# Kernel optimization log

Hardware: AMD Instinct MI355X
Metric: run time of the kernel (lower is better)

Reference implementation:

```python
import math
import jax, jax.numpy as jnp
import numpy as np

B = 16; ENC_S = 64; ENC_T = 96
SCALE = 64; POOL = 16; DM = 256; NH = 16
E_LAYERS = 3; D_LAYERS = 2; DFF = 1024
OUT_S = 64; OUT_T = 32
LN_EPS = 1e-5


def _pe(d_model, length):
    pos = np.arange(length, dtype=np.float32)[:, None]
    div = np.exp(np.arange(0, d_model, 2, dtype=np.float32) * (-math.log(10000.0) / d_model))
    pe = np.zeros((length, d_model), np.float32)
    pe[:, 0::2] = np.sin(pos * div)
    pe[:, 1::2] = np.cos(pos * div)
    return jnp.asarray(pe)


def _conv1d_circ(x, w, b):
    # x: (N, C, L), w: (O, C, 3); torch Conv1d(padding=1, padding_mode='circular')
    xp = jnp.pad(x, ((0, 0), (0, 0), (1, 1)), mode='wrap')
    y = jax.lax.conv_general_dilated(xp, w, (1,), 'VALID',
                                     dimension_numbers=('NCH', 'OIH', 'NCH'))
    return y + b[None, :, None]


def _layernorm(x, w, b):
    mu = jnp.mean(x, -1, keepdims=True)
    var = jnp.var(x, -1, keepdims=True)
    return (x - mu) * jax.lax.rsqrt(var + LN_EPS) * w + b


def _data_embedding(x, sproj_w, sproj_b, scproj_w, scproj_b, tok_w, tok_b):
    Bb = x.shape[0]
    h = _conv1d_circ(jnp.swapaxes(x, 1, 2), sproj_w, sproj_b)       # (B, enc_t, enc_t)
    h = _conv1d_circ(h, scproj_w, scproj_b)                          # (B, scale, enc_t)
    h = _conv1d_circ(jnp.swapaxes(h, 1, 2), scproj_w, scproj_b)     # (B, scale, scale)
    h = h.reshape(Bb * SCALE, 1, SCALE)
    tok = jnp.swapaxes(_conv1d_circ(h, tok_w, tok_b), 1, 2)          # (B*scale, scale, dm)
    emb = tok + _pe(DM, SCALE)[None]
    return emb.reshape(Bb, SCALE, SCALE, DM)


def _lin_attn(q, k, v, causal):
    # q,k,v: (Bp, L, H, E); k/v adaptively avg-pooled over L to POOL (L % POOL == 0)
    Bp, L, H, E = q.shape
    win = L // POOL
    kp = k.reshape(Bp, POOL, win, H, E).mean(axis=2)
    vp = v.reshape(Bp, POOL, win, H, E).mean(axis=2)
    scores = jnp.einsum('blhe,bshe->bhls', q, kp)      # (Bp, H, L, POOL)
    if causal:
        m = jnp.arange(POOL)[None, :] > jnp.arange(L)[:, None]
        scores = jnp.where(m[None, None], -jnp.inf, scores)
    A = jax.nn.softmax(scores / math.sqrt(E), axis=-1)
    return jnp.einsum('bhls,bshd->blhd', A, vp)


def _st_attn(x, kv, Wq, bq, Wo, bo, causal):
    Bb, T, S, dm = x.shape
    H = NH // 2
    proj = lambda z: z @ Wq.T + bq
    # faithful to source: query_projection used for q, k AND v; views are flat reshapes
    qt = proj(x.reshape(Bb * S, T, dm)).reshape(Bb * S, T, H, -1)
    qs = proj(x.reshape(Bb * T, S, dm)).reshape(Bb * T, S, H, -1)
    kt = proj(kv.reshape(Bb * S, T, dm)).reshape(Bb * S, T, H, -1)
    ks = proj(kv.reshape(Bb * T, S, dm)).reshape(Bb * T, S, H, -1)
    out_t = _lin_attn(qt, kt, kt, causal).reshape(Bb, S, T, -1)
    out_s = _lin_attn(qs, ks, ks, causal).reshape(Bb, S, T, -1)
    out = jnp.concatenate([out_t, out_s], axis=-1).reshape(Bb, S * T, 2 * dm)
    out = out @ Wo.T + bo
    return out.reshape(Bb, T, S, dm)


def _ffn(x, c1w, c1b, c2w, c2b):
    # conv1d kernel_size=1 over the T axis of (B*S, T, dm) == pointwise GEMM
    Bb, T, S, dm = x.shape
    y = x.reshape(Bb * S, T, dm)
    y = jax.nn.gelu(jnp.einsum('ntd,fd->ntf', y, c1w) + c1b, approximate=False)
    y = jnp.einsum('ntf,df->ntd', y, c2w) + c2b
    return y.reshape(Bb, T, S, dm)


def _forward(x_enc, x_dec,
             enc_sproj_w, enc_sproj_b, enc_scproj_w, enc_scproj_b, enc_tok_w, enc_tok_b,
             dec_sproj_w, dec_sproj_b, dec_scproj_w, dec_scproj_b, dec_tok_w, dec_tok_b,
             e_Wq, e_bq, e_Wo, e_bo, e_c1w, e_c1b, e_c2w, e_c2b,
             e_ln1w, e_ln1b, e_ln2w, e_ln2b, enc_norm_w, enc_norm_b,
             d_sWq, d_sbq, d_sWo, d_sbo, d_cWq, d_cbq, d_cWo, d_cbo,
             d_c1w, d_c1b, d_c2w, d_c2b,
             d_ln1w, d_ln1b, d_ln2w, d_ln2b, d_ln3w, d_ln3b,
             dec_norm_w, dec_norm_b, proj_w, proj_b):
    enc = _data_embedding(x_enc, enc_sproj_w, enc_sproj_b, enc_scproj_w, enc_scproj_b, enc_tok_w, enc_tok_b)
    for i in range(E_LAYERS):
        h = enc + _st_attn(enc, enc, e_Wq[i], e_bq[i], e_Wo[i], e_bo[i], False)
        h = _layernorm(h, e_ln1w[i], e_ln1b[i])
        enc = _layernorm(h + _ffn(h, e_c1w[i], e_c1b[i], e_c2w[i], e_c2b[i]), e_ln2w[i], e_ln2b[i])
    enc = _layernorm(enc, enc_norm_w, enc_norm_b)
    dec = _data_embedding(x_dec, dec_sproj_w, dec_sproj_b, dec_scproj_w, dec_scproj_b, dec_tok_w, dec_tok_b)
    for i in range(D_LAYERS):
        h = dec + _st_attn(dec, dec, d_sWq[i], d_sbq[i], d_sWo[i], d_sbo[i], True)
        h = _layernorm(h, d_ln1w[i], d_ln1b[i])
        h = h + _st_attn(h, enc, d_cWq[i], d_cbq[i], d_cWo[i], d_cbo[i], False)
        h = _layernorm(h, d_ln2w[i], d_ln2b[i])
        dec = _layernorm(h + _ffn(h, d_c1w[i], d_c1b[i], d_c2w[i], d_c2b[i]), d_ln3w[i], d_ln3b[i])
    dec = _layernorm(dec, dec_norm_w, dec_norm_b)
    dec = dec.mean(axis=2)                 # (B, scale, dm)
    out = dec @ proj_w.T + proj_b          # (B, scale, out_s)
    return out[:, -OUT_T:, :]


def setup_inputs() -> dict:
    keys = iter(jax.random.split(jax.random.key(0), 80))
    def nrm(shape, s=0.02):
        return jax.random.normal(next(keys), shape, jnp.float32) * s
    E, D = E_LAYERS, D_LAYERS
    inp = {
        'x_enc': nrm((B, ENC_T, ENC_S), 1.0),
        'x_dec': nrm((B, ENC_T, ENC_S), 1.0),
    }
    for p in ('enc', 'dec'):
        inp[p + '_sproj_w'] = nrm((ENC_T, ENC_S, 3)); inp[p + '_sproj_b'] = nrm((ENC_T,))
        inp[p + '_scproj_w'] = nrm((SCALE, ENC_T, 3)); inp[p + '_scproj_b'] = nrm((SCALE,))
        inp[p + '_tok_w'] = nrm((DM, 1, 3), 0.1); inp[p + '_tok_b'] = nrm((DM,))
    inp.update(
        e_Wq=nrm((E, DM, DM)), e_bq=nrm((E, DM)),
        e_Wo=nrm((E, DM, 2 * DM)), e_bo=nrm((E, DM)),
        e_c1w=nrm((E, DFF, DM)), e_c1b=nrm((E, DFF)),
        e_c2w=nrm((E, DM, DFF)), e_c2b=nrm((E, DM)),
        e_ln1w=jnp.ones((E, DM)), e_ln1b=jnp.zeros((E, DM)),
        e_ln2w=jnp.ones((E, DM)), e_ln2b=jnp.zeros((E, DM)),
        enc_norm_w=jnp.ones((DM,)), enc_norm_b=jnp.zeros((DM,)),
        d_sWq=nrm((D, DM, DM)), d_sbq=nrm((D, DM)),
        d_sWo=nrm((D, DM, 2 * DM)), d_sbo=nrm((D, DM)),
        d_cWq=nrm((D, DM, DM)), d_cbq=nrm((D, DM)),
        d_cWo=nrm((D, DM, 2 * DM)), d_cbo=nrm((D, DM)),
        d_c1w=nrm((D, DFF, DM)), d_c1b=nrm((D, DFF)),
        d_c2w=nrm((D, DM, DFF)), d_c2b=nrm((D, DM)),
        d_ln1w=jnp.ones((D, DM)), d_ln1b=jnp.zeros((D, DM)),
        d_ln2w=jnp.ones((D, DM)), d_ln2b=jnp.zeros((D, DM)),
        d_ln3w=jnp.ones((D, DM)), d_ln3b=jnp.zeros((D, DM)),
        dec_norm_w=jnp.ones((DM,)), dec_norm_b=jnp.zeros((DM,)),
        proj_w=nrm((OUT_S, DM)), proj_b=nrm((OUT_S,)),
    )
    return inp


def reference(x_enc, x_dec,
              enc_sproj_w, enc_sproj_b, enc_scproj_w, enc_scproj_b, enc_tok_w, enc_tok_b,
              dec_sproj_w, dec_sproj_b, dec_scproj_w, dec_scproj_b, dec_tok_w, dec_tok_b,
              e_Wq, e_bq, e_Wo, e_bo, e_c1w, e_c1b, e_c2w, e_c2b,
              e_ln1w, e_ln1b, e_ln2w, e_ln2b, enc_norm_w, enc_norm_b,
              d_sWq, d_sbq, d_sWo, d_sbo, d_cWq, d_cbq, d_cWo, d_cbo,
              d_c1w, d_c1b, d_c2w, d_c2b,
              d_ln1w, d_ln1b, d_ln2w, d_ln2b, d_ln3w, d_ln3b,
              dec_norm_w, dec_norm_b, proj_w, proj_b):
    return _forward(x_enc, x_dec,
                    enc_sproj_w, enc_sproj_b, enc_scproj_w, enc_scproj_b, enc_tok_w, enc_tok_b,
                    dec_sproj_w, dec_sproj_b, dec_scproj_w, dec_scproj_b, dec_tok_w, dec_tok_b,
                    e_Wq, e_bq, e_Wo, e_bo, e_c1w, e_c1b, e_c2w, e_c2b,
                    e_ln1w, e_ln1b, e_ln2w, e_ln2b, enc_norm_w, enc_norm_b,
                    d_sWq, d_sbq, d_sWo, d_sbo, d_cWq, d_cbq, d_cWo, d_cbo,
                    d_c1w, d_c1b, d_c2w, d_c2b,
                    d_ln1w, d_ln1b, d_ln2w, d_ln2b, d_ln3w, d_ln3b,
                    dec_norm_w, dec_norm_b, proj_w, proj_b)
```

## Files before the change

kernel.cpp:

```cpp
#include <hip/hip_runtime.h>


typedef unsigned short u16;
typedef short s16;
typedef __attribute__((ext_vector_type(8))) s16 bfrag;
typedef __attribute__((ext_vector_type(4))) float f32x4;

__device__ __forceinline__ float b2f(u16 u) {
  union { float f; unsigned int i; } v; v.i = ((unsigned int)u) << 16; return v.f;
}
__device__ __forceinline__ u16 f2b(float f) {
  union { float f; unsigned int i; } v; v.f = f;
  unsigned int x = v.i;
  return (u16)((x + 0x7FFFu + ((x >> 16) & 1u)) >> 16);
}
__device__ __forceinline__ float gelu_f(float v) {
  float u = 0.7978845608f * v * (1.0f + 0.044715f * v * v);
  float e = __expf(2.0f * u);
  return v * (1.0f - 1.0f / (e + 1.0f));
}

__device__ __forceinline__ void gload16(const void* g, void* l) {
  __builtin_amdgcn_global_load_lds(
      (const __attribute__((address_space(1))) unsigned int*)g,
      (__attribute__((address_space(3))) unsigned int*)l, 16, 0, 0);
}

__global__ void ws_signal(float* out, float v) { out[0] = v; }

__global__ void cvt_bf(const float* __restrict__ src, u16* __restrict__ dst, int n) {
  int i = blockIdx.x * 256 + threadIdx.x;
  if (i < n) dst[i] = f2b(src[i]);
}
__global__ void weff_bf(const float* __restrict__ Wo, u16* __restrict__ W) {
  int n = blockIdx.x, k = threadIdx.x;
  W[n * 256 + k] = f2b(Wo[n * 512 + k] + Wo[n * 512 + 256 + k]);
}

__global__ void pe_kernel(float* __restrict__ pe) {
  int l = blockIdx.x, d = threadIdx.x;
  int i = d >> 1;
  float div = expf((float)(2 * i) * (-9.210340371976184f / 256.0f));
  float ang = (float)l * div;
  pe[l * 256 + d] = (d & 1) ? cosf(ang) : sinf(ang);
}

__global__ void conv_sproj(const float* __restrict__ x, const float* __restrict__ w,
                           const float* __restrict__ bias, float* __restrict__ h1) {
  int o = blockIdx.x, b = blockIdx.y, l = threadIdx.x;
  const float* wo = w + o * 192;
  const float* xb = x + (size_t)b * 96 * 64;
  float acc = bias[o];
#pragma unroll
  for (int k = 0; k < 3; ++k) {
    int lp = l + k - 1; if (lp < 0) lp += 96; if (lp >= 96) lp -= 96;
    const float* xr = xb + lp * 64;
    for (int c = 0; c < 64; ++c) acc = fmaf(xr[c], wo[c * 3 + k], acc);
  }
  h1[((size_t)b * 96 + o) * 96 + l] = acc;
}

__global__ void conv_scproj_t(const float* __restrict__ h1, const float* __restrict__ w,
                              const float* __restrict__ bias, float* __restrict__ h2) {
  int o = blockIdx.x, b = blockIdx.y, l = threadIdx.x;
  const float* wo = w + o * 288;
  const float* hb = h1 + (size_t)b * 96 * 96;
  float acc = bias[o];
#pragma unroll
  for (int k = 0; k < 3; ++k) {
    int lp = l + k - 1; if (lp < 0) lp += 96; if (lp >= 96) lp -= 96;
    for (int c = 0; c < 96; ++c) acc = fmaf(hb[c * 96 + lp], wo[c * 3 + k], acc);
  }
  h2[((size_t)b * 64 + o) * 96 + l] = acc;
}

__global__ void conv_scproj_s(const float* __restrict__ h2, const float* __restrict__ w,
                              const float* __restrict__ bias, float* __restrict__ h3) {
  int o = blockIdx.x, b = blockIdx.y, l = threadIdx.x;
  const float* wo = w + o * 288;
  const float* hb = h2 + (size_t)b * 64 * 96;
  float acc = bias[o];
#pragma unroll
  for (int k = 0; k < 3; ++k) {
    int lp = l + k - 1; if (lp < 0) lp += 64; if (lp >= 64) lp -= 64;
    for (int c = 0; c < 96; ++c) acc = fmaf(hb[lp * 96 + c], wo[c * 3 + k], acc);
  }
  h3[((size_t)b * 64 + o) * 64 + l] = acc;
}

__global__ void tok_embed(const float* __restrict__ h3, const float* __restrict__ w,
                          const float* __restrict__ bias, const float* __restrict__ pe,
                          u16* __restrict__ E) {
  int g = blockIdx.x, d = threadIdx.x;
  __shared__ float row[64];
  if (d < 64) row[d] = h3[(size_t)g * 64 + d];
  __syncthreads();
  float w0 = w[d * 3], w1 = w[d * 3 + 1], w2 = w[d * 3 + 2], bd = bias[d];
  for (int j = 0; j < 64; ++j) {
    int jm = (j + 63) & 63, jp = (j + 1) & 63;
    float v = bd + row[jm] * w0 + row[j] * w1 + row[jp] * w2 + pe[j * 256 + d];
    E[((size_t)g * 64 + j) * 256 + d] = f2b(v);
  }
}

template <int ACT, int NBX>
__global__ __launch_bounds__(256) void mfma_gemm(const u16* __restrict__ A,
                                                 const u16* __restrict__ W,
                                                 const float* __restrict__ bias,
                                                 u16* __restrict__ C, int N, int K,
                                                 int nby) {
  __shared__ s16 smem[16384];
  s16* A0 = smem;        s16* A1 = smem + 4096;
  s16* B0 = smem + 8192; s16* B1 = smem + 12288;
  constexpr int LB = (NBX == 8) ? 3 : 1;
  int f = blockIdx.x;
  int q = (NBX * nby) >> 3;
  int w = (f & 7) * q + (f >> 3);
  int bx = w & (NBX - 1), by = w >> LB;
  int t = threadIdx.x;
  int wave = t >> 6, lane = t & 63;
  int wr = wave >> 1, wc = wave & 1;
  int row0 = by * 128, col0 = bx * 128;
  int kc = (lane >> 4) & 3, rr = lane & 15;
  const u16* Ap0 = A + (size_t)(row0 + wave * 16 + rr) * K + kc * 8;
  const u16* Ap1 = A + (size_t)(row0 + (wave + 4) * 16 + rr) * K + kc * 8;
  const u16* Bp0 = W + (size_t)(col0 + wave * 16 + rr) * K + kc * 8;
  const u16* Bp1 = W + (size_t)(col0 + (wave + 4) * 16 + rr) * K + kc * 8;
  f32x4 acc[4][4];
#pragma unroll
  for (int m = 0; m < 4; ++m)
#pragma unroll
    for (int n = 0; n < 4; ++n) acc[m][n] = (f32x4){0.f, 0.f, 0.f, 0.f};

  auto STAGE = [&](s16* a, s16* b, int kidx) {
    int k0 = kidx * 32;
    gload16(Ap0 + k0, a + wave * 512);
    gload16(Ap1 + k0, a + (wave + 4) * 512);
    gload16(Bp0 + k0, b + wave * 512);
    gload16(Bp1 + k0, b + (wave + 4) * 512);
  };
  int nk = K >> 5;
  auto STEP = [&](const s16* a, const s16* b, s16* sa, s16* sb, int ks) {
    if (ks + 1 < nk) asm volatile("s_waitcnt vmcnt(4)" ::: "memory");
    else             asm volatile("s_waitcnt vmcnt(0)" ::: "memory");
    __builtin_amdgcn_sched_barrier(0);
    __builtin_amdgcn_s_barrier();
    __builtin_amdgcn_sched_barrier(0);
    bfrag af[4], bf[4];
#pragma unroll
    for (int m = 0; m < 4; ++m) af[m] = *(const bfrag*)(a + ((wr * 4 + m) * 64 + lane) * 8);
#pragma unroll
    for (int n = 0; n < 4; ++n) bf[n] = *(const bfrag*)(b + ((wc * 4 + n) * 64 + lane) * 8);
    asm volatile("s_waitcnt lgkmcnt(0)" ::: "memory");
    __builtin_amdgcn_sched_barrier(0);
    __builtin_amdgcn_s_barrier();
    __builtin_amdgcn_sched_barrier(0);
    if (ks + 2 < nk) STAGE(sa, sb, ks + 2);
#pragma unroll
    for (int m = 0; m < 4; ++m)
#pragma unroll
      for (int n = 0; n < 4; ++n)
        acc[m][n] = __builtin_amdgcn_mfma_f32_16x16x32_bf16(af[m], bf[n], acc[m][n], 0, 0, 0);
  };

  STAGE(A0, B0, 0);
  STAGE(A1, B1, 1);
  for (int ks = 0; ks < nk; ks += 2) {
    STEP(A0, B0, A0, B0, ks);
    STEP(A1, B1, A1, B1, ks + 1);
  }
  s16* Cs = smem;
  int g4 = (lane >> 4) << 2;
  int cl = lane & 15;
  float bc[4];
#pragma unroll
  for (int n = 0; n < 4; ++n) bc[n] = bias[col0 + wc * 64 + n * 16 + cl];
#pragma unroll
  for (int P = 0; P < 4; ++P) {
    __syncthreads();
    if (wr == (P >> 1)) {
#pragma unroll
      for (int mm = 0; mm < 2; ++mm) {
        int m = (P & 1) * 2 + mm;
#pragma unroll
        for (int n = 0; n < 4; ++n) {
#pragma unroll
          for (int r = 0; r < 4; ++r) {
            float v = acc[m][n][r] + bc[n];
            if (ACT == 1) v = gelu_f(v);
            Cs[(mm * 16 + g4 + r) * 136 + wc * 64 + n * 16 + cl] = (s16)f2b(v);
          }
        }
      }
    }
    __syncthreads();
#pragma unroll
    for (int it = 0; it < 2; ++it) {
      int idx = it * 256 + t;
      int lr = idx >> 4, slot = idx & 15;
      *(uint4*)(C + (size_t)(row0 + P * 32 + lr) * N + col0 + slot * 8) =
          *(const uint4*)(Cs + lr * 136 + slot * 8);
    }
  }
}

__global__ __launch_bounds__(512) void mfma_gemm_resln(const u16* __restrict__ X,
                                                       const u16* __restrict__ W,
                                                       const float* __restrict__ bias,
                                                       u16* __restrict__ R,
                                                       const float* __restrict__ lnw,
                                                       const float* __restrict__ lnb,
                                                       int K) {
  __shared__ s16 smem[24576];
  __shared__ float pls[32][4][2];
  s16* A0 = smem;        s16* A1 = smem + 4096;
  s16* B0 = smem + 8192; s16* B1 = smem + 16384;
  int t = threadIdx.x;
  int wave = t >> 6, lane = t & 63;
  int wr = wave >> 2, wc = wave & 3;
  int row0 = blockIdx.x * 128;
  int kc = (lane >> 4) & 3, rr = lane & 15;
  const u16* Xp = X + (size_t)(row0 + wave * 16 + rr) * K + kc * 8;
  const u16* Wp0 = W + (size_t)(wave * 16 + rr) * K + kc * 8;
  const u16* Wp1 = W + (size_t)((wave + 8) * 16 + rr) * K + kc * 8;
  f32x4 acc[4][4];
#pragma unroll
  for (int m = 0; m < 4; ++m)
#pragma unroll
    for (int n = 0; n < 4; ++n) acc[m][n] = (f32x4){0.f, 0.f, 0.f, 0.f};

  auto STAGE = [&](s16* a, s16* b, int kidx) {
    int k0 = kidx * 32;
    gload16(Xp + k0, a + wave * 512);
    gload16(Wp0 + k0, b + wave * 512);
    gload16(Wp1 + k0, b + (wave + 8) * 512);
  };
  int nk = K >> 5;
  auto STEP = [&](const s16* a, const s16* b, s16* sa, s16* sb, int ks) {
    if (ks + 1 < nk) asm volatile("s_waitcnt vmcnt(3)" ::: "memory");
    else             asm volatile("s_waitcnt vmcnt(0)" ::: "memory");
    __builtin_amdgcn_sched_barrier(0);
    __builtin_amdgcn_s_barrier();
    __builtin_amdgcn_sched_barrier(0);
    bfrag af[4], bf[4];
#pragma unroll
    for (int m = 0; m < 4; ++m) af[m] = *(const bfrag*)(a + ((wr * 4 + m) * 64 + lane) * 8);
#pragma unroll
    for (int n = 0; n < 4; ++n) bf[n] = *(const bfrag*)(b + ((wc * 4 + n) * 64 + lane) * 8);
    asm volatile("s_waitcnt lgkmcnt(0)" ::: "memory");
    __builtin_amdgcn_sched_barrier(0);
    __builtin_amdgcn_s_barrier();
    __builtin_amdgcn_sched_barrier(0);
    if (ks + 2 < nk) STAGE(sa, sb, ks + 2);
#pragma unroll
    for (int m = 0; m < 4; ++m)
#pragma unroll
      for (int n = 0; n < 4; ++n)
        acc[m][n] = __builtin_amdgcn_mfma_f32_16x16x32_bf16(af[m], bf[n], acc[m][n], 0, 0, 0);
  };

  STAGE(A0, B0, 0);
  STAGE(A1, B1, 1);
  for (int ks = 0; ks < nk; ks += 2) {
    STEP(A0, B0, A0, B0, ks);
    STEP(A1, B1, A1, B1, ks + 1);
  }
  s16* Rs = smem;
  int g4 = (lane >> 4) << 2;
  int cl = lane & 15;
  float lw[4], lb[4], bc[4];
#pragma unroll
  for (int n = 0; n < 4; ++n) {
    int col = wc * 64 + n * 16 + cl;
    bc[n] = bias[col]; lw[n] = lnw[col]; lb[n] = lnb[col];
  }
#pragma unroll
  for (int P = 0; P < 4; ++P) {
    bool own = (wr == (P >> 1));
    __syncthreads();
#pragma unroll
    for (int it = 0; it < 2; ++it) {
      int idx = it * 512 + t;
      int lr = idx >> 5, slot = idx & 31;
      *(uint4*)(Rs + lr * 264 + slot * 8) =
          *(const uint4*)(R + (size_t)(row0 + P * 32 + lr) * 256 + slot * 8);
    }
    __syncthreads();
    if (own) {
#pragma unroll
      for (int mm = 0; mm < 2; ++mm) {
        int m = (P & 1) * 2 + mm;
#pragma unroll
        for (int r = 0; r < 4; ++r) {
          int lr = mm * 16 + g4 + r;
          float s = 0.f, s2 = 0.f;
#pragma unroll
          for (int n = 0; n < 4; ++n) {
            float v = acc[m][n][r] + bc[n] +
                      b2f((u16)Rs[lr * 264 + wc * 64 + n * 16 + cl]);
            acc[m][n][r] = v;
            s += v; s2 = fmaf(v, v, s2);
          }
#pragma unroll
          for (int o = 1; o < 16; o <<= 1) { s += __shfl_xor(s, o); s2 += __shfl_xor(s2, o); }
          if (cl == 0) { pls[lr][wc][0] = s; pls[lr][wc][1] = s2; }
        }
      }
    }
    __syncthreads();
    if (own) {
#pragma unroll
      for (int mm = 0; mm < 2; ++mm) {
        int m = (P & 1) * 2 + mm;
#pragma unroll
        for (int r = 0; r < 4; ++r) {
          int lr = mm * 16 + g4 + r;
          float s = pls[lr][0][0] + pls[lr][1][0] + pls[lr][2][0] + pls[lr][3][0];
          float s2 = pls[lr][0][1] + pls[lr][1][1] + pls[lr][2][1] + pls[lr][3][1];
          float mu = s * (1.0f / 256.0f);
          float var = fmaxf(s2 * (1.0f / 256.0f) - mu * mu, 0.0f);
          float rs = rsqrtf(var + 1e-5f);
#pragma unroll
          for (int n = 0; n < 4; ++n) {
            Rs[lr * 264 + wc * 64 + n * 16 + cl] =
                (s16)f2b((acc[m][n][r] - mu) * rs * lw[n] + lb[n]);
          }
        }
      }
    }
    __syncthreads();
#pragma unroll
    for (int it = 0; it < 2; ++it) {
      int idx = it * 512 + t;
      int lr = idx >> 5, slot = idx & 31;
      *(uint4*)(R + (size_t)(row0 + P * 32 + lr) * 256 + slot * 8) =
          *(const uint4*)(Rs + lr * 264 + slot * 8);
    }
  }
}

template <int CROSS, int CAUSAL>
__global__ __launch_bounds__(512) void lin_attn(u16* __restrict__ Q,
                                                const u16* __restrict__ KP) {
  __shared__ u16 qs[64 * 264];
  __shared__ float kpool[16][260];
  int p = blockIdx.x, t = threadIdx.x;
  u16* Qg = Q + (size_t)p * 16384;
#pragma unroll
  for (int i = 0; i < 4; ++i) {
    int idx = i * 512 + t;
    int row = idx >> 5, slot = idx & 31;
    *(uint4*)(qs + row * 264 + slot * 8) = *(const uint4*)(Qg + row * 256 + slot * 8);
  }
  __syncthreads();
  if (CROSS) {
    for (int idx = t; idx < 4096; idx += 512) {
      int s = idx >> 8, d = idx & 255;
      kpool[s][d] = b2f(KP[((size_t)p * 16 + s) * 256 + d]);
    }
  } else {
    for (int idx = t; idx < 4096; idx += 512) {
      int s = idx >> 8, d = idx & 255;
      const u16* b0 = qs + (4 * s) * 264 + d;
      kpool[s][d] = 0.25f * (b2f(b0[0]) + b2f(b0[264]) + b2f(b0[528]) + b2f(b0[792]));
    }
  }
  __syncthreads();
  int h = t >> 6, l = t & 63;
  u16* q = qs + l * 264 + h * 32;
  float qr[32];
#pragma unroll
  for (int e = 0; e < 32; e += 4) {
    ushort4 v = *(const ushort4*)&q[e];
    qr[e] = b2f(v.x); qr[e + 1] = b2f(v.y); qr[e + 2] = b2f(v.z); qr[e + 3] = b2f(v.w);
  }
  float sc[16], mx = -INFINITY;
#pragma unroll
  for (int s = 0; s < 16; ++s) {
    const float* kp = &kpool[s][h * 32];
    float d = 0.f;
#pragma unroll
    for (int e = 0; e < 32; ++e) d = fmaf(qr[e], kp[e], d);
    d *= 0.17677669529663687f;
    if (CAUSAL && s > l) d = -INFINITY;
    sc[s] = d; mx = fmaxf(mx, d);
  }
  float sum = 0.f;
#pragma unroll
  for (int s = 0; s < 16; ++s) { sc[s] = expf(sc[s] - mx); sum += sc[s]; }
  float inv = 1.0f / sum;
  float o[32] = {};
#pragma unroll
  for (int s = 0; s < 16; ++s) {
    float a = sc[s] * inv;
    const float* vp = &kpool[s][h * 32];
#pragma unroll
    for (int e = 0; e < 32; ++e) o[e] = fmaf(a, vp[e], o[e]);
  }
#pragma unroll
  for (int e = 0; e < 32; e += 4) {
    ushort4 v;
    v.x = f2b(o[e]); v.y = f2b(o[e + 1]); v.z = f2b(o[e + 2]); v.w = f2b(o[e + 3]);
    *(ushort4*)&q[e] = v;
  }
  __syncthreads();
#pragma unroll
  for (int i = 0; i < 4; ++i) {
    int idx = i * 512 + t;
    int row = idx >> 5, slot = idx & 31;
    *(uint4*)(Qg + row * 256 + slot * 8) = *(const uint4*)(qs + row * 264 + slot * 8);
  }
}

__global__ __launch_bounds__(256) void ln_bf(u16* __restrict__ X,
                                             const float* __restrict__ w,
                                             const float* __restrict__ b) {
  int lane = threadIdx.x & 63, wv = threadIdx.x >> 6;
  size_t row = (size_t)blockIdx.x * 4 + wv;
  size_t off = row * 256 + lane * 4;
  ushort4 xv = *(const ushort4*)(X + off);
  float v0 = b2f(xv.x), v1 = b2f(xv.y), v2 = b2f(xv.z), v3 = b2f(xv.w);
  float s = v0 + v1 + v2 + v3;
  float s2 = v0 * v0 + v1 * v1 + v2 * v2 + v3 * v3;
#pragma unroll
  for (int o = 32; o; o >>= 1) { s += __shfl_xor(s, o); s2 += __shfl_xor(s2, o); }
  float mu = s * (1.0f / 256.0f);
  float var = fmaxf(s2 * (1.0f / 256.0f) - mu * mu, 0.0f);
  float rs = rsqrtf(var + 1e-5f);
  float4 w4 = *(const float4*)(w + lane * 4);
  float4 b4 = *(const float4*)(b + lane * 4);
  ushort4 o4;
  o4.x = f2b((v0 - mu) * rs * w4.x + b4.x);
  o4.y = f2b((v1 - mu) * rs * w4.y + b4.y);
  o4.z = f2b((v2 - mu) * rs * w4.z + b4.z);
  o4.w = f2b((v3 - mu) * rs * w4.w + b4.w);
  *(ushort4*)(X + off) = o4;
}

__global__ void pool_bf(const u16* __restrict__ A, u16* __restrict__ P) {
  int r = blockIdx.x, d = threadIdx.x;
  int g = r >> 4, s = r & 15;
  const u16* src = A + ((size_t)g * 64 + 4 * (size_t)s) * 256 + d;
  float v = 0.25f * (b2f(src[0]) + b2f(src[256]) + b2f(src[512]) + b2f(src[768]));
  P[(size_t)r * 256 + d] = f2b(v);
}

__global__ __launch_bounds__(256) void mean_proj_bf(const u16* __restrict__ X,
                                                    const float* __restrict__ pw,
                                                    const float* __restrict__ pb,
                                                    float* __restrict__ out) {
  int bid = blockIdx.x;
  int b = bid >> 5, ii = bid & 31;
  int i = 32 + ii;
  __shared__ float md[256];
  int d = threadIdx.x;
  const u16* base = X + ((size_t)b * 64 + i) * 64 * 256 + d;
  float s = 0.f;
  for (int j = 0; j < 64; ++j) s += b2f(base[(size_t)j * 256]);
  md[d] = s * (1.0f / 64.0f);
  __syncthreads();
  if (d < 64) {
    float acc = pb[d];
    const float* wr = pw + d * 256;
    for (int k = 0; k < 256; ++k) acc = fmaf(md[k], wr[k], acc);
    out[((size_t)b * 32 + ii) * 64 + d] = acc;
  }
}

extern "C" void kernel_launch(void* const* d_in, const int* in_sizes, int n_in,
                              void* d_out, int out_size, void* d_ws, size_t ws_size,
                              hipStream_t stream) {
  (void)in_sizes; (void)out_size;
  if (n_in < 50) return;

  const float* x_enc = (const float*)d_in[0];
  const float* x_dec = (const float*)d_in[1];
  const float* enc_sproj_w = (const float*)d_in[2];
  const float* enc_sproj_b = (const float*)d_in[3];
  const float* enc_scproj_w = (const float*)d_in[4];
  const float* enc_scproj_b = (const float*)d_in[5];
  const float* enc_tok_w = (const float*)d_in[6];
  const float* enc_tok_b = (const float*)d_in[7];
  const float* dec_sproj_w = (const float*)d_in[8];
  const float* dec_sproj_b = (const float*)d_in[9];
  const float* dec_scproj_w = (const float*)d_in[10];
  const float* dec_scproj_b = (const float*)d_in[11];
  const float* dec_tok_w = (const float*)d_in[12];
  const float* dec_tok_b = (const float*)d_in[13];
  const float* e_Wq = (const float*)d_in[14];
  const float* e_bq = (const float*)d_in[15];
  const float* e_Wo = (const float*)d_in[16];
  const float* e_bo = (const float*)d_in[17];
  const float* e_c1w = (const float*)d_in[18];
  const float* e_c1b = (const float*)d_in[19];
  const float* e_c2w = (const float*)d_in[20];
  const float* e_c2b = (const float*)d_in[21];
  const float* e_ln1w = (const float*)d_in[22];
  const float* e_ln1b = (const float*)d_in[23];
  const float* e_ln2w = (const float*)d_in[24];
  const float* e_ln2b = (const float*)d_in[25];
  const float* enc_norm_w = (const float*)d_in[26];
  const float* enc_norm_b = (const float*)d_in[27];
  const float* d_sWq = (const float*)d_in[28];
  const float* d_sbq = (const float*)d_in[29];
  const float* d_sWo = (const float*)d_in[30];
  const float* d_sbo = (const float*)d_in[31];
  const float* d_cWq = (const float*)d_in[32];
  const float* d_cbq = (const float*)d_in[33];
  const float* d_cWo = (const float*)d_in[34];
  const float* d_cbo = (const float*)d_in[35];
  const float* d_c1w = (const float*)d_in[36];
  const float* d_c1b = (const float*)d_in[37];
  const float* d_c2w = (const float*)d_in[38];
  const float* d_c2b = (const float*)d_in[39];
  const float* d_ln1w = (const float*)d_in[40];
  const float* d_ln1b = (const float*)d_in[41];
  const float* d_ln2w = (const float*)d_in[42];
  const float* d_ln2b = (const float*)d_in[43];
  const float* d_ln3w = (const float*)d_in[44];
  const float* d_ln3b = (const float*)d_in[45];
  const float* dec_norm_w = (const float*)d_in[46];
  const float* dec_norm_b = (const float*)d_in[47];
  const float* proj_w = (const float*)d_in[48];
  const float* proj_b = (const float*)d_in[49];

  const size_t ACT = 16777216;
  const size_t POOLE = 4194304;
  const size_t WBN = 3538944;
  size_t base_need = (3 * ACT + 2 * POOLE + WBN) * 2 +
                     (size_t)(16384 + 147456 + 98304 + 65536) * 4;
  if (ws_size < base_need) {
    ws_signal<<<1, 1, 0, stream>>>((float*)d_out, (float)(ws_size >> 20));
    return;
  }
  char* wsb = (char*)d_ws;
  u16* A_enc = (u16*)wsb;  wsb += ACT * 2;
  u16* A_dec = (u16*)wsb;  wsb += ACT * 2;
  u16* T1 = (u16*)wsb;     wsb += ACT * 2;
  u16* PA = (u16*)wsb;     wsb += POOLE * 2;
  u16* PK = (u16*)wsb;     wsb += POOLE * 2;
  u16* WB = (u16*)wsb;     wsb += WBN * 2;
  float* PE = (float*)wsb;  wsb += 16384 * 4;
  float* EH1 = (float*)wsb; wsb += 147456 * 4;
  float* EH2 = (float*)wsb; wsb += 98304 * 4;
  float* EH3 = (float*)wsb; wsb += 65536 * 4;

  int hf_rows = 16384;
  u16* HF = T1;
  if (ws_size >= base_need + (size_t)65536 * 1024 * 2) {
    hf_rows = 65536; HF = (u16*)wsb;
  } else if (ws_size >= base_need + (size_t)32768 * 1024 * 2) {
    hf_rows = 32768; HF = (u16*)wsb;
  }

  u16* eWq = WB;
  u16* eWeff = WB + 196608;
  u16* eC1 = WB + 393216;
  u16* eC2 = WB + 1179648;
  u16* dB = WB + 1966080;
  u16* dsWq = dB;
  u16* dsWeff = dB + 131072;
  u16* dcWq = dB + 262144;
  u16* dcWeff = dB + 393216;
  u16* dC1 = dB + 524288;
  u16* dC2 = dB + 1048576;

  cvt_bf<<<768, 256, 0, stream>>>(e_Wq, eWq, 196608);
  cvt_bf<<<3072, 256, 0, stream>>>(e_c1w, eC1, 786432);
  cvt_bf<<<3072, 256, 0, stream>>>(e_c2w, eC2, 786432);
  cvt_bf<<<512, 256, 0, stream>>>(d_sWq, dsWq, 131072);
  cvt_bf<<<512, 256, 0, stream>>>(d_cWq, dcWq, 131072);
  cvt_bf<<<2048, 256, 0, stream>>>(d_c1w, dC1, 524288);
  cvt_bf<<<2048, 256, 0, stream>>>(d_c2w, dC2, 524288);
  for (int i = 0; i < 3; ++i)
    weff_bf<<<256, 256, 0, stream>>>(e_Wo + (size_t)i * 131072, eWeff + (size_t)i * 65536);
  for (int i = 0; i < 2; ++i) {
    weff_bf<<<256, 256, 0, stream>>>(d_sWo + (size_t)i * 131072, dsWeff + (size_t)i * 65536);
    weff_bf<<<256, 256, 0, stream>>>(d_cWo + (size_t)i * 131072, dcWeff + (size_t)i * 65536);
  }

  pe_kernel<<<64, 256, 0, stream>>>(PE);

  conv_sproj<<<dim3(96, 16), 96, 0, stream>>>(x_enc, enc_sproj_w, enc_sproj_b, EH1);
  conv_scproj_t<<<dim3(64, 16), 96, 0, stream>>>(EH1, enc_scproj_w, enc_scproj_b, EH2);
  conv_scproj_s<<<dim3(64, 16), 64, 0, stream>>>(EH2, enc_scproj_w, enc_scproj_b, EH3);
  tok_embed<<<1024, 256, 0, stream>>>(EH3, enc_tok_w, enc_tok_b, PE, A_enc);

  for (int i = 0; i < 3; ++i) {
    mfma_gemm<0, 2><<<1024, 256, 0, stream>>>(A_enc, eWq + (size_t)i * 65536,
                                              e_bq + i * 256, T1, 256, 256, 512);
    lin_attn<0, 0><<<1024, 512, 0, stream>>>(T1, nullptr);
    mfma_gemm_resln<<<512, 512, 0, stream>>>(T1, eWeff + (size_t)i * 65536, e_bo + i * 256,
                                             A_enc, e_ln1w + i * 256, e_ln1b + i * 256, 256);
    for (int m0 = 0; m0 < 65536; m0 += hf_rows) {
      u16* Xc = A_enc + (size_t)m0 * 256;
      int nby = hf_rows / 128;
      mfma_gemm<1, 8><<<8 * nby, 256, 0, stream>>>(
          Xc, eC1 + (size_t)i * 262144, e_c1b + i * 1024, HF, 1024, 256, nby);
      mfma_gemm_resln<<<nby, 512, 0, stream>>>(
          HF, eC2 + (size_t)i * 262144, e_c2b + i * 256, Xc,
          e_ln2w + i * 256, e_ln2b + i * 256, 1024);
    }
  }
  ln_bf<<<16384, 256, 0, stream>>>(A_enc, enc_norm_w, enc_norm_b);
  pool_bf<<<16384, 256, 0, stream>>>(A_enc, PA);

  conv_sproj<<<dim3(96, 16), 96, 0, stream>>>(x_dec, dec_sproj_w, dec_sproj_b, EH1);
  conv_scproj_t<<<dim3(64, 16), 96, 0, stream>>>(EH1, dec_scproj_w, dec_scproj_b, EH2);
  conv_scproj_s<<<dim3(64, 16), 64, 0, stream>>>(EH2, dec_scproj_w, dec_scproj_b, EH3);
  tok_embed<<<1024, 256, 0, stream>>>(EH3, dec_tok_w, dec_tok_b, PE, A_dec);

  for (int i = 0; i < 2; ++i) {
    mfma_gemm<0, 2><<<1024, 256, 0, stream>>>(A_dec, dsWq + (size_t)i * 65536,
                                              d_sbq + i * 256, T1, 256, 256, 512);
    lin_attn<0, 1><<<1024, 512, 0, stream>>>(T1, nullptr);
    mfma_gemm_resln<<<512, 512, 0, stream>>>(T1, dsWeff + (size_t)i * 65536, d_sbo + i * 256,
                                             A_dec, d_ln1w + i * 256, d_ln1b + i * 256, 256);
    mfma_gemm<0, 2><<<1024, 256, 0, stream>>>(A_dec, dcWq + (size_t)i * 65536,
                                              d_cbq + i * 256, T1, 256, 256, 512);
    mfma_gemm<0, 2><<<256, 256, 0, stream>>>(PA, dcWq + (size_t)i * 65536,
                                             d_cbq + i * 256, PK, 256, 256, 128);
    lin_attn<1, 0><<<1024, 512, 0, stream>>>(T1, PK);
    mfma_gemm_resln<<<512, 512, 0, stream>>>(T1, dcWeff + (size_t)i * 65536, d_cbo + i * 256,
                                             A_dec, d_ln2w + i * 256, d_ln2b + i * 256, 256);
    for (int m0 = 0; m0 < 65536; m0 += hf_rows) {
      u16* Xc = A_dec + (size_t)m0 * 256;
      int nby = hf_rows / 128;
      mfma_gemm<1, 8><<<8 * nby, 256, 0, stream>>>(
          Xc, dC1 + (size_t)i * 262144, d_c1b + i * 1024, HF, 1024, 256, nby);
      mfma_gemm_resln<<<nby, 512, 0, stream>>>(
          HF, dC2 + (size_t)i * 262144, d_c2b + i * 256, Xc,
          d_ln3w + i * 256, d_ln3b + i * 256, 1024);
    }
  }
  ln_bf<<<16384, 256, 0, stream>>>(A_dec, dec_norm_w, dec_norm_b);

  mean_proj_bf<<<512, 256, 0, stream>>>(A_dec, proj_w, proj_b, (float*)d_out);
}
```

Baseline: 1.792 ms.

## Restructure GEMM main loop to process K=64 per barrier step

```diff
diff --git a/kernel.cpp b/kernel.cpp
--- a/kernel.cpp
+++ b/kernel.cpp
@@ -109,9 +109,8 @@
                                                  const float* __restrict__ bias,
                                                  u16* __restrict__ C, int N, int K,
                                                  int nby) {
-  __shared__ s16 smem[16384];
-  s16* A0 = smem;        s16* A1 = smem + 4096;
-  s16* B0 = smem + 8192; s16* B1 = smem + 12288;
+  __shared__ s16 As[8192];
+  __shared__ s16 Bs[8192];
   constexpr int LB = (NBX == 8) ? 3 : 1;
   int f = blockIdx.x;
   int q = (NBX * nby) >> 3;
@@ -132,44 +131,53 @@
 #pragma unroll
     for (int n = 0; n < 4; ++n) acc[m][n] = (f32x4){0.f, 0.f, 0.f, 0.f};
 
-  auto STAGE = [&](s16* a, s16* b, int kidx) {
-    int k0 = kidx * 32;
+  auto STAGE32 = [&](s16* a, s16* b, int kidx32) {
+    int k0 = kidx32 * 32;
     gload16(Ap0 + k0, a + wave * 512);
     gload16(Ap1 + k0, a + (wave + 4) * 512);
     gload16(Bp0 + k0, b + wave * 512);
     gload16(Bp1 + k0, b + (wave + 4) * 512);
   };
-  int nk = K >> 5;
-  auto STEP = [&](const s16* a, const s16* b, s16* sa, s16* sb, int ks) {
-    if (ks + 1 < nk) asm volatile("s_waitcnt vmcnt(4)" ::: "memory");
-    else             asm volatile("s_waitcnt vmcnt(0)" ::: "memory");
+  auto STAGE64 = [&](int kidx64) {
+    STAGE32(As, Bs, kidx64 * 2);
+    STAGE32(As + 4096, Bs + 4096, kidx64 * 2 + 1);
+  };
+
+  int nk = K >> 6;
+  STAGE64(0);
+  for (int ks = 0; ks < nk; ++ks) {
+    asm volatile("s_waitcnt vmcnt(0)" ::: "memory");
     __builtin_amdgcn_sched_barrier(0);
     __builtin_amdgcn_s_barrier();
     __builtin_amdgcn_sched_barrier(0);
-    bfrag af[4], bf[4];
-#pragma unroll
-    for (int m = 0; m < 4; ++m) af[m] = *(const bfrag*)(a + ((wr * 4 + m) * 64 + lane) * 8);
-#pragma unroll
-    for (int n = 0; n < 4; ++n) bf[n] = *(const bfrag*)(b + ((wc * 4 + n) * 64 + lane) * 8);
+    bfrag al[4], bl[4], ah[4], bh[4];
+#pragma unroll
+    for (int m = 0; m < 4; ++m) {
+      al[m] = *(const bfrag*)(As + ((wr * 4 + m) * 64 + lane) * 8);
+      ah[m] = *(const bfrag*)(As + 4096 + ((wr * 4 + m) * 64 + lane) * 8);
+    }
+#pragma unroll
+    for (int n = 0; n < 4; ++n) {
+      bl[n] = *(const bfrag*)(Bs + ((wc * 4 + n) * 64 + lane) * 8);
+      bh[n] = *(const bfrag*)(Bs + 4096 + ((wc * 4 + n) * 64 + lane) * 8);
+    }
     asm volatile("s_waitcnt lgkmcnt(0)" ::: "memory");
     __builtin_amdgcn_sched_barrier(0);
     __builtin_amdgcn_s_barrier();
     __builtin_amdgcn_sched_barrier(0);
-    if (ks + 2 < nk) STAGE(sa, sb, ks + 2);
+    if (ks + 1 < nk) STAGE64(ks + 1);
 #pragma unroll
     for (int m = 0; m < 4; ++m)
 #pragma unroll
       for (int n = 0; n < 4; ++n)
-        acc[m][n] = __builtin_amdgcn_mfma_f32_16x16x32_bf16(af[m], bf[n], acc[m][n], 0, 0, 0);
-  };
-
-  STAGE(A0, B0, 0);
-  STAGE(A1, B1, 1);
-  for (int ks = 0; ks < nk; ks += 2) {
-    STEP(A0, B0, A0, B0, ks);
-    STEP(A1, B1, A1, B1, ks + 1);
-  }
-  s16* Cs = smem;
+        acc[m][n] = __builtin_amdgcn_mfma_f32_16x16x32_bf16(al[m], bl[n], acc[m][n], 0, 0, 0);
+#pragma unroll
+    for (int m = 0; m < 4; ++m)
+#pragma unroll
+      for (int n = 0; n < 4; ++n)
+        acc[m][n] = __builtin_amdgcn_mfma_f32_16x16x32_bf16(ah[m], bh[n], acc[m][n], 0, 0, 0);
+  }
+  s16* Cs = As;
   int g4 = (lane >> 4) << 2;
   int cl = lane & 15;
   float bc[4];
```

Result: slower. 1.840 ms (+2.7%).

## Fuse Q projection GEMM into linear attention and batch prologue kernels

Applied to the files above, without the earlier changes.

```diff
diff --git a/kernel.cpp b/kernel.cpp
--- a/kernel.cpp
+++ b/kernel.cpp
@@ -28,13 +28,30 @@
 
 __global__ void ws_signal(float* out, float v) { out[0] = v; }
 
-__global__ void cvt_bf(const float* __restrict__ src, u16* __restrict__ dst, int n) {
+__global__ void cvt_all(const float* s0, const float* s1, const float* s2,
+                        const float* s3, const float* s4, const float* s5,
+                        const float* s6,
+                        u16* d0, u16* d1, u16* d2, u16* d3, u16* d4, u16* d5,
+                        u16* d6,
+                        int n0, int n1, int n2, int n3, int n4, int n5, int n6) {
+  const float* S[7] = {s0, s1, s2, s3, s4, s5, s6};
+  u16* D[7] = {d0, d1, d2, d3, d4, d5, d6};
+  int N[7] = {n0, n1, n2, n3, n4, n5, n6};
+  int j = blockIdx.y;
   int i = blockIdx.x * 256 + threadIdx.x;
-  if (i < n) dst[i] = f2b(src[i]);
-}
-__global__ void weff_bf(const float* __restrict__ Wo, u16* __restrict__ W) {
+  if (i < N[j]) D[j][i] = f2b(S[j][i]);
+}
+
+__global__ void weff_all(const float* s0, const float* s1, const float* s2,
+                         const float* s3, const float* s4, const float* s5,
+                         const float* s6,
+                         u16* d0, u16* d1, u16* d2, u16* d3, u16* d4, u16* d5,
+                         u16* d6) {
+  const float* S[7] = {s0, s1, s2, s3, s4, s5, s6};
+  u16* D[7] = {d0, d1, d2, d3, d4, d5, d6};
+  int j = blockIdx.y;
   int n = blockIdx.x, k = threadIdx.x;
-  W[n * 256 + k] = f2b(Wo[n * 512 + k] + Wo[n * 512 + 256 + k]);
+  D[j][n * 256 + k] = f2b(S[j][n * 512 + k] + S[j][n * 512 + 256 + k]);
 }
 
 __global__ void pe_kernel(float* __restrict__ pe) {
@@ -45,12 +62,19 @@
   pe[l * 256 + d] = (d & 1) ? cosf(ang) : sinf(ang);
 }
 
-__global__ void conv_sproj(const float* __restrict__ x, const float* __restrict__ w,
-                           const float* __restrict__ bias, float* __restrict__ h1) {
-  int o = blockIdx.x, b = blockIdx.y, l = threadIdx.x;
+__global__ void conv_sproj(const float* xe, const float* xd,
+                           const float* we, const float* be,
+                           const float* wd, const float* bd,
+                           float* h1e, float* h1d) {
+  int o = blockIdx.x, bb = blockIdx.y, l = threadIdx.x;
+  int b = (bb < 16) ? bb : bb - 16;
+  const float* x = (bb < 16) ? xe : xd;
+  const float* w = (bb < 16) ? we : wd;
+  const float* bi = (bb < 16) ? be : bd;
+  float* h1 = (bb < 16) ? h1e : h1d;
   const float* wo = w + o * 192;
   const float* xb = x + (size_t)b * 96 * 64;
-  float acc = bias[o];
+  float acc = bi[o];
 #pragma unroll
   for (int k = 0; k < 3; ++k) {
     int lp = l + k - 1; if (lp < 0) lp += 96; if (lp >= 96) lp -= 96;
@@ -60,12 +84,19 @@
   h1[((size_t)b * 96 + o) * 96 + l] = acc;
 }
 
-__global__ void conv_scproj_t(const float* __restrict__ h1, const float* __restrict__ w,
-                              const float* __restrict__ bias, float* __restrict__ h2) {
-  int o = blockIdx.x, b = blockIdx.y, l = threadIdx.x;
+__global__ void conv_scproj_t(const float* h1e, const float* h1d,
+                              const float* we, const float* be,
+                              const float* wd, const float* bd,
+                              float* h2e, float* h2d) {
+  int o = blockIdx.x, bb = blockIdx.y, l = threadIdx.x;
+  int b = (bb < 16) ? bb : bb - 16;
+  const float* h1 = (bb < 16) ? h1e : h1d;
+  const float* w = (bb < 16) ? we : wd;
+  const float* bi = (bb < 16) ? be : bd;
+  float* h2 = (bb < 16) ? h2e : h2d;
   const float* wo = w + o * 288;
   const float* hb = h1 + (size_t)b * 96 * 96;
-  float acc = bias[o];
+  float acc = bi[o];
 #pragma unroll
   for (int k = 0; k < 3; ++k) {
     int lp = l + k - 1; if (lp < 0) lp += 96; if (lp >= 96) lp -= 96;
@@ -74,12 +105,19 @@
   h2[((size_t)b * 64 + o) * 96 + l] = acc;
 }
 
-__global__ void conv_scproj_s(const float* __restrict__ h2, const float* __restrict__ w,
-                              const float* __restrict__ bias, float* __restrict__ h3) {
-  int o = blockIdx.x, b = blockIdx.y, l = threadIdx.x;
+__global__ void conv_scproj_s(const float* h2e, const float* h2d,
+                              const float* we, const float* be,
+                              const float* wd, const float* bd,
+                              float* h3e, float* h3d) {
+  int o = blockIdx.x, bb = blockIdx.y, l = threadIdx.x;
+  int b = (bb < 16) ? bb : bb - 16;
+  const float* h2 = (bb < 16) ? h2e : h2d;
+  const float* w = (bb < 16) ? we : wd;
+  const float* bi = (bb < 16) ? be : bd;
+  float* h3 = (bb < 16) ? h3e : h3d;
   const float* wo = w + o * 288;
   const float* hb = h2 + (size_t)b * 64 * 96;
-  float acc = bias[o];
+  float acc = bi[o];
 #pragma unroll
   for (int k = 0; k < 3; ++k) {
     int lp = l + k - 1; if (lp < 0) lp += 64; if (lp >= 64) lp -= 64;
@@ -88,17 +126,24 @@
   h3[((size_t)b * 64 + o) * 64 + l] = acc;
 }
 
-__global__ void tok_embed(const float* __restrict__ h3, const float* __restrict__ w,
-                          const float* __restrict__ bias, const float* __restrict__ pe,
-                          u16* __restrict__ E) {
-  int g = blockIdx.x, d = threadIdx.x;
+__global__ void tok_embed(const float* h3e, const float* h3d,
+                          const float* we, const float* be,
+                          const float* wd, const float* bd,
+                          const float* __restrict__ pe,
+                          u16* Ee, u16* Ed) {
+  int gg = blockIdx.x, d = threadIdx.x;
+  int g = (gg < 1024) ? gg : gg - 1024;
+  const float* h3 = (gg < 1024) ? h3e : h3d;
+  const float* w = (gg < 1024) ? we : wd;
+  const float* bi = (gg < 1024) ? be : bd;
+  u16* E = (gg < 1024) ? Ee : Ed;
   __shared__ float row[64];
   if (d < 64) row[d] = h3[(size_t)g * 64 + d];
   __syncthreads();
-  float w0 = w[d * 3], w1 = w[d * 3 + 1], w2 = w[d * 3 + 2], bd = bias[d];
+  float w0 = w[d * 3], w1 = w[d * 3 + 1], w2 = w[d * 3 + 2], bd_ = bi[d];
   for (int j = 0; j < 64; ++j) {
     int jm = (j + 63) & 63, jp = (j + 1) & 63;
-    float v = bd + row[jm] * w0 + row[j] * w1 + row[jp] * w2 + pe[j * 256 + d];
+    float v = bd_ + row[jm] * w0 + row[j] * w1 + row[jp] * w2 + pe[j * 256 + d];
     E[((size_t)g * 64 + j) * 256 + d] = f2b(v);
   }
 }
@@ -340,75 +385,128 @@
 }
 
 template <int CROSS, int CAUSAL>
-__global__ __launch_bounds__(512) void lin_attn(u16* __restrict__ Q,
-                                                const u16* __restrict__ KP) {
-  __shared__ u16 qs[64 * 264];
-  __shared__ float kpool[16][260];
+__global__ __launch_bounds__(256) void qk_attn(const u16* __restrict__ A,
+                                               const u16* __restrict__ Wq,
+                                               const float* __restrict__ bq,
+                                               u16* __restrict__ O,
+                                               const u16* __restrict__ KP) {
+  __shared__ s16 smem[27136];
+  s16* Qs = smem;
+  s16* As = smem + 16896;
+  s16* Bs = smem + 18944;
+  float* kp = (float*)(smem + 16896);
   int p = blockIdx.x, t = threadIdx.x;
-  u16* Qg = Q + (size_t)p * 16384;
-#pragma unroll
-  for (int i = 0; i < 4; ++i) {
-    int idx = i * 512 + t;
-    int row = idx >> 5, slot = idx & 31;
-    *(uint4*)(qs + row * 264 + slot * 8) = *(const uint4*)(Qg + row * 256 + slot * 8);
+  int wave = t >> 6, lane = t & 63;
+  int wr = wave >> 1, wc = wave & 1;
+  int kc = (lane >> 4) & 3, rr = lane & 15;
+  const u16* Ap = A + (size_t)(p * 64 + wave * 16 + rr) * 256 + kc * 8;
+  const u16* Wp = Wq + (size_t)rr * 256 + kc * 8;
+  f32x4 acc[2][8];
+#pragma unroll
+  for (int m = 0; m < 2; ++m)
+#pragma unroll
+    for (int n = 0; n < 8; ++n) acc[m][n] = (f32x4){0.f, 0.f, 0.f, 0.f};
+
+#pragma unroll
+  for (int ks = 0; ks < 8; ++ks) {
+    int k0 = ks * 32;
+    gload16(Ap + k0, As + wave * 512);
+#pragma unroll
+    for (int i = 0; i < 4; ++i) {
+      int fb = wave + i * 4;
+      gload16(Wp + (size_t)fb * 16 * 256 + k0, Bs + fb * 512);
+    }
+    __syncthreads();
+    bfrag a[2], b[8];
+#pragma unroll
+    for (int m = 0; m < 2; ++m) a[m] = *(const bfrag*)(As + ((wr * 2 + m) * 64 + lane) * 8);
+#pragma unroll
+    for (int n = 0; n < 8; ++n) b[n] = *(const bfrag*)(Bs + ((wc * 8 + n) * 64 + lane) * 8);
+#pragma unroll
+    for (int m = 0; m < 2; ++m)
+#pragma unroll
+      for (int n = 0; n < 8; ++n)
+        acc[m][n] = __builtin_amdgcn_mfma_f32_16x16x32_bf16(a[m], b[n], acc[m][n], 0, 0, 0);
+    __syncthreads();
+  }
+  int g4 = (lane >> 4) << 2;
+  int cl = lane & 15;
+#pragma unroll
+  for (int m = 0; m < 2; ++m) {
+#pragma unroll
+    for (int n = 0; n < 8; ++n) {
+      int col = wc * 128 + n * 16 + cl;
+      float bcol = bq[col];
+#pragma unroll
+      for (int r = 0; r < 4; ++r) {
+        int row = wr * 32 + m * 16 + g4 + r;
+        Qs[row * 264 + col] = (s16)f2b(acc[m][n][r] + bcol);
+      }
+    }
   }
   __syncthreads();
   if (CROSS) {
-    for (int idx = t; idx < 4096; idx += 512) {
+    for (int idx = t; idx < 4096; idx += 256) {
       int s = idx >> 8, d = idx & 255;
-      kpool[s][d] = b2f(KP[((size_t)p * 16 + s) * 256 + d]);
+      kp[s * 260 + d] = b2f(KP[((size_t)p * 16 + s) * 256 + d]);
     }
   } else {
-    for (int idx = t; idx < 4096; idx += 512) {
+    for (int idx = t; idx < 4096; idx += 256) {
       int s = idx >> 8, d = idx & 255;
-      const u16* b0 = qs + (4 * s) * 264 + d;
-      kpool[s][d] = 0.25f * (b2f(b0[0]) + b2f(b0[264]) + b2f(b0[528]) + b2f(b0[792]));
+      const s16* b0 = Qs + (4 * s) * 264 + d;
+      kp[s * 260 + d] = 0.25f * (b2f((u16)b0[0]) + b2f((u16)b0[264]) +
+                                 b2f((u16)b0[528]) + b2f((u16)b0[792]));
     }
   }
   __syncthreads();
-  int h = t >> 6, l = t & 63;
-  u16* q = qs + l * 264 + h * 32;
-  float qr[32];
-#pragma unroll
-  for (int e = 0; e < 32; e += 4) {
-    ushort4 v = *(const ushort4*)&q[e];
-    qr[e] = b2f(v.x); qr[e + 1] = b2f(v.y); qr[e + 2] = b2f(v.z); qr[e + 3] = b2f(v.w);
-  }
-  float sc[16], mx = -INFINITY;
-#pragma unroll
-  for (int s = 0; s < 16; ++s) {
-    const float* kp = &kpool[s][h * 32];
-    float d = 0.f;
-#pragma unroll
-    for (int e = 0; e < 32; ++e) d = fmaf(qr[e], kp[e], d);
-    d *= 0.17677669529663687f;
-    if (CAUSAL && s > l) d = -INFINITY;
-    sc[s] = d; mx = fmaxf(mx, d);
-  }
-  float sum = 0.f;
-#pragma unroll
-  for (int s = 0; s < 16; ++s) { sc[s] = expf(sc[s] - mx); sum += sc[s]; }
-  float inv = 1.0f / sum;
-  float o[32] = {};
-#pragma unroll
-  for (int s = 0; s < 16; ++s) {
-    float a = sc[s] * inv;
-    const float* vp = &kpool[s][h * 32];
-#pragma unroll
-    for (int e = 0; e < 32; ++e) o[e] = fmaf(a, vp[e], o[e]);
-  }
-#pragma unroll
-  for (int e = 0; e < 32; e += 4) {
-    ushort4 v;
-    v.x = f2b(o[e]); v.y = f2b(o[e + 1]); v.z = f2b(o[e + 2]); v.w = f2b(o[e + 3]);
-    *(ushort4*)&q[e] = v;
+#pragma unroll
+  for (int pi = 0; pi < 2; ++pi) {
+    int pp = t + pi * 256;
+    int h = pp >> 6, l = pp & 63;
+    s16* q = Qs + l * 264 + h * 32;
+    float qr[32];
+#pragma unroll
+    for (int e = 0; e < 32; e += 4) {
+      ushort4 v = *(const ushort4*)&q[e];
+      qr[e] = b2f(v.x); qr[e + 1] = b2f(v.y); qr[e + 2] = b2f(v.z); qr[e + 3] = b2f(v.w);
+    }
+    float sc[16], mx = -INFINITY;
+#pragma unroll
+    for (int s = 0; s < 16; ++s) {
+      const float* kpp = kp + s * 260 + h * 32;
+      float d = 0.f;
+#pragma unroll
+      for (int e = 0; e < 32; ++e) d = fmaf(qr[e], kpp[e], d);
+      d *= 0.17677669529663687f;
+      if (CAUSAL && s > l) d = -INFINITY;
+      sc[s] = d; mx = fmaxf(mx, d);
+    }
+    float sum = 0.f;
+#pragma unroll
+    for (int s = 0; s < 16; ++s) { sc[s] = expf(sc[s] - mx); sum += sc[s]; }
+    float inv = 1.0f / sum;
+    float o[32] = {};
+#pragma unroll
+    for (int s = 0; s < 16; ++s) {
+      float a = sc[s] * inv;
+      const float* vp = kp + s * 260 + h * 32;
+#pragma unroll
+      for (int e = 0; e < 32; ++e) o[e] = fmaf(a, vp[e], o[e]);
+    }
+#pragma unroll
+    for (int e = 0; e < 32; e += 4) {
+      ushort4 v;
+      v.x = f2b(o[e]); v.y = f2b(o[e + 1]); v.z = f2b(o[e + 2]); v.w = f2b(o[e + 3]);
+      *(ushort4*)&q[e] = v;
+    }
   }
   __syncthreads();
-#pragma unroll
-  for (int i = 0; i < 4; ++i) {
-    int idx = i * 512 + t;
+  u16* Og = O + (size_t)p * 16384;
+#pragma unroll
+  for (int i = 0; i < 8; ++i) {
+    int idx = i * 256 + t;
     int row = idx >> 5, slot = idx & 31;
-    *(uint4*)(Qg + row * 256 + slot * 8) = *(const uint4*)(qs + row * 264 + slot * 8);
+    *(uint4*)(Og + row * 256 + slot * 8) = *(const uint4*)(Qs + row * 264 + slot * 8);
   }
 }
 
@@ -528,7 +626,7 @@
   const size_t POOLE = 4194304;
   const size_t WBN = 3538944;
   size_t base_need = (3 * ACT + 2 * POOLE + WBN) * 2 +
-                     (size_t)(16384 + 147456 + 98304 + 65536) * 4;
+                     (size_t)(16384 + 2 * (147456 + 98304 + 65536)) * 4;
   if (ws_size < base_need) {
     ws_signal<<<1, 1, 0, stream>>>((float*)d_out, (float)(ws_size >> 20));
     return;
@@ -544,6 +642,9 @@
   float* EH1 = (float*)wsb; wsb += 147456 * 4;
   float* EH2 = (float*)wsb; wsb += 98304 * 4;
   float* EH3 = (float*)wsb; wsb += 65536 * 4;
+  float* FH1 = (float*)wsb; wsb += 147456 * 4;
+  float* FH2 = (float*)wsb; wsb += 98304 * 4;
+  float* FH3 = (float*)wsb; wsb += 65536 * 4;
 
   int hf_rows = 16384;
   u16* HF = T1;
@@ -565,31 +666,30 @@
   u16* dC1 = dB + 524288;
   u16* dC2 = dB + 1048576;
 
-  cvt_bf<<<768, 256, 0, stream>>>(e_Wq, eWq, 196608);
-  cvt_bf<<<3072, 256, 0, stream>>>(e_c1w, eC1, 786432);
-  cvt_bf<<<3072, 256, 0, stream>>>(e_c2w, eC2, 786432);
-  cvt_bf<<<512, 256, 0, stream>>>(d_sWq, dsWq, 131072);
-  cvt_bf<<<512, 256, 0, stream>>>(d_cWq, dcWq, 131072);
-  cvt_bf<<<2048, 256, 0, stream>>>(d_c1w, dC1, 524288);
-  cvt_bf<<<2048, 256, 0, stream>>>(d_c2w, dC2, 524288);
-  for (int i = 0; i < 3; ++i)
-    weff_bf<<<256, 256, 0, stream>>>(e_Wo + (size_t)i * 131072, eWeff + (size_t)i * 65536);
-  for (int i = 0; i < 2; ++i) {
-    weff_bf<<<256, 256, 0, stream>>>(d_sWo + (size_t)i * 131072, dsWeff + (size_t)i * 65536);
-    weff_bf<<<256, 256, 0, stream>>>(d_cWo + (size_t)i * 131072, dcWeff + (size_t)i * 65536);
-  }
+  cvt_all<<<dim3(3072, 7), 256, 0, stream>>>(
+      e_Wq, e_c1w, e_c2w, d_sWq, d_cWq, d_c1w, d_c2w,
+      eWq, eC1, eC2, dsWq, dcWq, dC1, dC2,
+      196608, 786432, 786432, 131072, 131072, 524288, 524288);
+  weff_all<<<dim3(256, 7), 256, 0, stream>>>(
+      e_Wo, e_Wo + 131072, e_Wo + 262144, d_sWo, d_sWo + 131072,
+      d_cWo, d_cWo + 131072,
+      eWeff, eWeff + 65536, eWeff + 131072, dsWeff, dsWeff + 65536,
+      dcWeff, dcWeff + 65536);
 
   pe_kernel<<<64, 256, 0, stream>>>(PE);
 
-  conv_sproj<<<dim3(96, 16), 96, 0, stream>>>(x_enc, enc_sproj_w, enc_sproj_b, EH1);
-  conv_scproj_t<<<dim3(64, 16), 96, 0, stream>>>(EH1, enc_scproj_w, enc_scproj_b, EH2);
-  conv_scproj_s<<<dim3(64, 16), 64, 0, stream>>>(EH2, enc_scproj_w, enc_scproj_b, EH3);
-  tok_embed<<<1024, 256, 0, stream>>>(EH3, enc_tok_w, enc_tok_b, PE, A_enc);
+  conv_sproj<<<dim3(96, 32), 96, 0, stream>>>(x_enc, x_dec, enc_sproj_w, enc_sproj_b,
+                                              dec_sproj_w, dec_sproj_b, EH1, FH1);
+  conv_scproj_t<<<dim3(64, 32), 96, 0, stream>>>(EH1, FH1, enc_scproj_w, enc_scproj_b,
+                                                 dec_scproj_w, dec_scproj_b, EH2, FH2);
+  conv_scproj_s<<<dim3(64, 32), 64, 0, stream>>>(EH2, FH2, enc_scproj_w, enc_scproj_b,
+                                                 dec_scproj_w, dec_scproj_b, EH3, FH3);
+  tok_embed<<<2048, 256, 0, stream>>>(EH3, FH3, enc_tok_w, enc_tok_b,
+                                      dec_tok_w, dec_tok_b, PE, A_enc, A_dec);
 
   for (int i = 0; i < 3; ++i) {
-    mfma_gemm<0, 2><<<1024, 256, 0, stream>>>(A_enc, eWq + (size_t)i * 65536,
-                                              e_bq + i * 256, T1, 256, 256, 512);
-    lin_attn<0, 0><<<1024, 512, 0, stream>>>(T1, nullptr);
+    qk_attn<0, 0><<<1024, 256, 0, stream>>>(A_enc, eWq + (size_t)i * 65536,
+                                            e_bq + i * 256, T1, nullptr);
     mfma_gemm_resln<<<512, 512, 0, stream>>>(T1, eWeff + (size_t)i * 65536, e_bo + i * 256,
                                              A_enc, e_ln1w + i * 256, e_ln1b + i * 256, 256);
     for (int m0 = 0; m0 < 65536; m0 += hf_rows) {
@@ -605,22 +705,15 @@
   ln_bf<<<16384, 256, 0, stream>>>(A_enc, enc_norm_w, enc_norm_b);
   pool_bf<<<16384, 256, 0, stream>>>(A_enc, PA);
 
-  conv_sproj<<<dim3(96, 16), 96, 0, stream>>>(x_dec, dec_sproj_w, dec_sproj_b, EH1);
-  conv_scproj_t<<<dim3(64, 16), 96, 0, stream>>>(EH1, dec_scproj_w, dec_scproj_b, EH2);
-  conv_scproj_s<<<dim3(64, 16), 64, 0, stream>>>(EH2, dec_scproj_w, dec_scproj_b, EH3);
-  tok_embed<<<1024, 256, 0, stream>>>(EH3, dec_tok_w, dec_tok_b, PE, A_dec);
-
   for (int i = 0; i < 2; ++i) {
-    mfma_gemm<0, 2><<<1024, 256, 0, stream>>>(A_dec, dsWq + (size_t)i * 65536,
-                                              d_sbq + i * 256, T1, 256, 256, 512);
-    lin_attn<0, 1><<<1024, 512, 0, stream>>>(T1, nullptr);
+    qk_attn<0, 1><<<1024, 256, 0, stream>>>(A_dec, dsWq + (size_t)i * 65536,
+                                            d_sbq + i * 256, T1, nullptr);
     mfma_gemm_resln<<<512, 512, 0, stream>>>(T1, dsWeff + (size_t)i * 65536, d_sbo + i * 256,
                                              A_dec, d_ln1w + i * 256, d_ln1b + i * 256, 256);
-    mfma_gemm<0, 2><<<1024, 256, 0, stream>>>(A_dec, dcWq + (size_t)i * 65536,
-                                              d_cbq + i * 256, T1, 256, 256, 512);
     mfma_gemm<0, 2><<<256, 256, 0, stream>>>(PA, dcWq + (size_t)i * 65536,
                                              d_cbq + i * 256, PK, 256, 256, 128);
-    lin_attn<1, 0><<<1024, 512, 0, stream>>>(T1, PK);
+    qk_attn<1, 0><<<1024, 256, 0, stream>>>(A_dec, dcWq + (size_t)i * 65536,
+                                            d_cbq + i * 256, T1, PK);
     mfma_gemm_resln<<<512, 512, 0, stream>>>(T1, dcWeff + (size_t)i * 65536, d_cbo + i * 256,
                                              A_dec, d_ln2w + i * 256, d_ln2b + i * 256, 256);
     for (int m0 = 0; m0 < 65536; m0 += hf_rows) {
```

After: 1.872 ms. +4.5%, slower.
